# Kernel optimization log

Hardware: AMD Instinct MI355X
Metric: run time of the kernel (lower is better)

## Reference

```python
import jax, jax.numpy as jnp
import numpy as np

D = 1024
H = 16
K = D // H
B = 2
S = 2048

def setup_inputs() -> dict:
    key = jax.random.key(0)
    k1, k2, k3, k4, k5 = jax.random.split(key, 5)
    x = jax.random.normal(k1, (B, S, D), dtype=jnp.float32)
    # nn.Linear(d, 3d): weight [3d, d], bias [3d]
    Wqkv = jax.random.normal(k2, (3 * D, D), dtype=jnp.float32) / np.sqrt(D)
    bqkv = jax.random.normal(k3, (3 * D,), dtype=jnp.float32) * 0.01
    Wproj = jax.random.normal(k4, (D, D), dtype=jnp.float32) / np.sqrt(D)
    bproj = jax.random.normal(k5, (D,), dtype=jnp.float32) * 0.01
    return {"x": x, "Wqkv": Wqkv, "bqkv": bqkv, "Wproj": Wproj, "bproj": bproj}

def reference(x, Wqkv, bqkv, Wproj, bproj):
    Bsz, Slen, d = x.shape
    # fused QKV projection: [B,S,3d] -> [B,S,3,H,K] -> (3, B, H, S, K)
    qkv = (jnp.einsum('bsd,ed->bse', x, Wqkv) + bqkv).reshape(Bsz, Slen, 3, H, K)
    q, k, v = jnp.moveaxis(qkv, 2, 0).transpose(0, 1, 3, 2, 4)
    scale = 1.0 / jnp.sqrt(jnp.asarray(K, dtype=x.dtype))
    scores = jnp.einsum('bhqk,bhmk->bhqm', q, k) * scale  # [B,H,S,S]
    a = jax.nn.softmax(scores, axis=-1)
    # dropout is identity in eval mode
    o = jnp.einsum('bhqm,bhmk->bhqk', a, v)  # [B,H,S,K]
    o = o.transpose(0, 2, 1, 3).reshape(Bsz, Slen, d)
    return jnp.einsum('bsd,ed->bse', o, Wproj) + bproj
```

## Files before the change

kernel.cpp:

```cpp
#include <hip/hip_runtime.h>
#include <cstdint>

typedef unsigned short ushort_t;
typedef short short8 __attribute__((ext_vector_type(8)));
typedef float f32x4 __attribute__((ext_vector_type(4)));
typedef float float4v __attribute__((ext_vector_type(4)));
typedef unsigned int uint2v __attribute__((ext_vector_type(2)));
typedef unsigned int uint4v __attribute__((ext_vector_type(4)));

#define DDIM 1024
#define HH 16
#define HEADK 64
#define BB 2
#define SS 2048

#if __has_builtin(__builtin_amdgcn_exp2f)
#define EXP2F(x) __builtin_amdgcn_exp2f(x)
#else
#define EXP2F(x) exp2f(x)
#endif

__device__ __forceinline__ ushort_t f2bf(float f) {
  union { float f; uint32_t u; } c; c.f = f;
  uint32_t u = c.u;
  u += 0x7fffu + ((u >> 16) & 1u);
  return (ushort_t)(u >> 16);
}

__device__ __forceinline__ uint32_t pkbf_trunc(float a, float b) {
  union { float f; uint32_t u; } ca, cb;
  ca.f = a; cb.f = b;
  return __builtin_amdgcn_perm(cb.u, ca.u, 0x07060302);
}

__device__ __forceinline__ uint32_t pkbf_rne(float a, float b) {
  return (uint32_t)f2bf(a) | ((uint32_t)f2bf(b) << 16);
}

__device__ __forceinline__ float bfhi2f(uint32_t u) {
  union { uint32_t u; float f; } c; c.u = u & 0xffff0000u; return c.f;
}
__device__ __forceinline__ float bflo2f(uint32_t u) {
  union { uint32_t u; float f; } c; c.u = u << 16; return c.f;
}

__device__ __forceinline__ void glds16(const ushort_t* gp, ushort_t* lp) {
  __builtin_amdgcn_global_load_lds(
      (const __attribute__((address_space(1))) uint32_t*)gp,
      (__attribute__((address_space(3))) uint32_t*)lp, 16, 0, 0);
}

__global__ void cvt3_kernel(const float* __restrict__ s0, ushort_t* __restrict__ d0, int n0,
                            const float* __restrict__ s1, ushort_t* __restrict__ d1, int n1,
                            const float* __restrict__ s2, ushort_t* __restrict__ d2, int n2) {
  int i = blockIdx.x * blockDim.x + threadIdx.x;
  const float* src; ushort_t* dst; int k;
  if (i < n0) { src = s0; dst = d0; k = i; }
  else if (i < n0 + n1) { src = s1; dst = d1; k = i - n0; }
  else if (i < n0 + n1 + n2) { src = s2; dst = d2; k = i - n0 - n1; }
  else return;
  float4v v = ((const float4v*)src)[k];
  uint2v o; o[0] = pkbf_rne(v[0], v[1]); o[1] = pkbf_rne(v[2], v[3]);
  ((uint2v*)dst)[k] = o;
}

__global__ __launch_bounds__(512, 2) void gemm_qkv(
    const ushort_t* __restrict__ A, const ushort_t* __restrict__ Bm,
    const float* __restrict__ bias, ushort_t* __restrict__ Cbf) {
  constexpr int Kd = 1024;
  __shared__ ushort_t smem[65536];
  const int tid = threadIdx.x;
  const int wv = tid >> 6, lane = tid & 63;
  const int l15 = lane & 15, quad = lane >> 4;
  const int wm = wv >> 2, wn = wv & 3;
  const int tm0 = blockIdx.y * 256, tn0 = blockIdx.x * 256;
  const int lrow = lane >> 3;
  const int gcb = (lane & 7) ^ lrow;

  f32x4 acc[8][4];
#pragma unroll
  for (int i = 0; i < 8; ++i)
#pragma unroll
    for (int j = 0; j < 4; ++j) acc[i][j] = (f32x4){0.f, 0.f, 0.f, 0.f};

  auto stage = [&](int t, int buf) {
    ushort_t* As = smem + buf * 32768;
    ushort_t* Bs = As + 16384;
    const int k0 = t * 64;
#pragma unroll
    for (int c = 0; c < 4; ++c) {
      int seg = wv * 4 + c;
      glds16(A + (size_t)(tm0 + seg * 8 + lrow) * Kd + k0 + gcb * 8,
             As + seg * 512);
      glds16(Bm + (size_t)(tn0 + seg * 8 + lrow) * Kd + k0 + gcb * 8,
             Bs + seg * 512);
    }
  };

  stage(0, 0);
  for (int t = 0; t < 16; ++t) {
    const int cur = t & 1;
    asm volatile("" ::: "memory");
    __builtin_amdgcn_s_barrier();
    if (t + 1 < 16) {
      stage(t + 1, cur ^ 1);
      asm volatile("s_waitcnt vmcnt(8)" ::: "memory");
    } else {
      asm volatile("s_waitcnt vmcnt(0)" ::: "memory");
    }
    __builtin_amdgcn_s_barrier();
    asm volatile("" ::: "memory");
    __builtin_amdgcn_sched_barrier(0);

    const ushort_t* As = smem + cur * 32768;
    const ushort_t* Bs = As + 16384;
    short8 bfr[4][2];
#pragma unroll
    for (int j = 0; j < 4; ++j)
#pragma unroll
      for (int kc = 0; kc < 2; ++kc) {
        int n = wn * 64 + j * 16 + l15;
        bfr[j][kc] =
            *(const short8*)(Bs + n * 64 + (((kc * 4 + quad) ^ (l15 & 7)) << 3));
      }
#pragma unroll
    for (int q = 0; q < 4; ++q) {
      short8 af[2][2];
#pragma unroll
      for (int i2 = 0; i2 < 2; ++i2)
#pragma unroll
        for (int kc = 0; kc < 2; ++kc) {
          int r = wm * 128 + (q * 2 + i2) * 16 + l15;
          af[i2][kc] =
              *(const short8*)(As + r * 64 + (((kc * 4 + quad) ^ (l15 & 7)) << 3));
        }
      __builtin_amdgcn_s_setprio(1);
#pragma unroll
      for (int kc = 0; kc < 2; ++kc)
#pragma unroll
        for (int i2 = 0; i2 < 2; ++i2)
#pragma unroll
          for (int j = 0; j < 4; ++j)
            acc[q * 2 + i2][j] = __builtin_amdgcn_mfma_f32_16x16x32_bf16(
                af[i2][kc], bfr[j][kc], acc[q * 2 + i2][j], 0, 0, 0);
      __builtin_amdgcn_s_setprio(0);
    }
  }

  const int tsel = tn0 >> 10;
  if (tsel < 2) {
#pragma unroll
    for (int j = 0; j < 4; ++j) {
      int col = tn0 + wn * 64 + j * 16 + l15;
      float bv = bias[col];
      int hh = (col >> 6) & 15, kk2 = col & 63;
#pragma unroll
      for (int mi = 0; mi < 8; ++mi) {
        int row0 = tm0 + wm * 128 + mi * 16 + quad * 4;
#pragma unroll
        for (int r = 0; r < 4; ++r) {
          int row = row0 + r;
          int b = row >> 11, s = row & 2047;
          float v = acc[mi][j][r] + bv;
          if (tsel == 0) v *= 0.18033688f;
          size_t base = (((size_t)tsel * BB + b) * HH + hh) * ((size_t)SS * HEADK);
          Cbf[base + (size_t)s * HEADK + kk2] = f2bf(v);
        }
      }
    }
  } else {
    __builtin_amdgcn_s_barrier();
    ushort_t* slab = smem + wv * 8192;
#pragma unroll
    for (int j = 0; j < 4; ++j) {
      int c = j * 16 + l15;
      float bv = bias[tn0 + wn * 64 + c];
#pragma unroll
      for (int mi = 0; mi < 8; ++mi) {
        int row0 = mi * 16 + quad * 4;
        uint2v dw;
        dw[0] = pkbf_rne(acc[mi][j][0] + bv, acc[mi][j][1] + bv);
        dw[1] = pkbf_rne(acc[mi][j][2] + bv, acc[mi][j][3] + bv);
        int rb = row0 >> 3;
        *(uint2v*)(&slab[c * 128 + (((rb ^ (c & 15)) << 3) | (row0 & 7))]) = dw;
      }
    }
    const int r2 = lane & 15, cg = lane >> 4;
#pragma unroll
    for (int it = 0; it < 16; ++it) {
      int c = it * 4 + cg;
      short8 vv = *(const short8*)(&slab[c * 128 + ((r2 ^ (c & 15)) << 3)]);
      int gcol = tn0 + wn * 64 + c;
      int hh = (gcol >> 6) & 15, kk2 = gcol & 63;
      int grow = tm0 + wm * 128 + r2 * 8;
      int b = grow >> 11, s = grow & 2047;
      size_t base = (((size_t)2 * BB + b) * HH + hh) * ((size_t)SS * HEADK);
      *(short8*)(&Cbf[base + (size_t)kk2 * SS + s]) = vv;
    }
  }
}

__global__ __launch_bounds__(512, 2) void gemm_proj(
    const ushort_t* __restrict__ Op0, const ushort_t* __restrict__ Op1,
    const float* __restrict__ Lp, const ushort_t* __restrict__ Bm,
    const float* __restrict__ bias, float* __restrict__ Cout) {
  constexpr int Kd = 1024;
  constexpr size_t nsL = (size_t)BB * HH * SS;
  __shared__ ushort_t smem[32768];
  const int tid = threadIdx.x;
  const int wv = tid >> 6, lane = tid & 63;
  const int l15 = lane & 15, quad = lane >> 4;
  const int wm = wv >> 2, wn = wv & 3;
  const int tm0 = blockIdx.y * 128, tn0 = blockIdx.x * 128;
  const int lrow = lane >> 3, gcb = (lane & 7) ^ lrow;

  const int ar = tid >> 2, acg = tid & 3;
  const int grow = tm0 + ar;
  const int ab = grow >> 11, as_ = grow & 2047;

  f32x4 acc[4][2];
#pragma unroll
  for (int i = 0; i < 4; ++i)
#pragma unroll
    for (int j = 0; j < 2; ++j) acc[i][j] = (f32x4){0.f, 0.f, 0.f, 0.f};

  uint4v ra0, ra1, rb0, rb1;
  float rl0, rl1;

  auto readA = [&](int t) {
    size_t lo = (size_t)(ab * HH + t) * SS + as_;
    size_t po = lo * 64 + acg * 16;
    ra0 = *(const uint4v*)(Op0 + po);
    ra1 = *(const uint4v*)(Op0 + po + 8);
    rb0 = *(const uint4v*)(Op1 + po);
    rb1 = *(const uint4v*)(Op1 + po + 8);
    rl0 = Lp[lo];
    rl1 = Lp[nsL + lo];
  };
  auto writeA = [&](int p) {
    float inv = 1.0f / (rl0 + rl1);
    uint4v olo, ohi;
#pragma unroll
    for (int d = 0; d < 4; ++d) {
      olo[d] = pkbf_rne((bflo2f(ra0[d]) + bflo2f(rb0[d])) * inv,
                        (bfhi2f(ra0[d]) + bfhi2f(rb0[d])) * inv);
      ohi[d] = pkbf_rne((bflo2f(ra1[d]) + bflo2f(rb1[d])) * inv,
                        (bfhi2f(ra1[d]) + bfhi2f(rb1[d])) * inv);
    }
    ushort_t* As = smem + p * 16384;
    *(uint4v*)(&As[ar * 64 + (((acg * 2) ^ (ar & 7)) << 3)]) = olo;
    *(uint4v*)(&As[ar * 64 + (((acg * 2 + 1) ^ (ar & 7)) << 3)]) = ohi;
  };
  auto stageB = [&](int t, int p) {
    ushort_t* Bs = smem + p * 16384 + 8192;
#pragma unroll
    for (int c = 0; c < 2; ++c) {
      int seg = wv * 2 + c;
      glds16(Bm + (size_t)(tn0 + seg * 8 + lrow) * Kd + t * 64 + gcb * 8,
             Bs + seg * 512);
    }
  };

  readA(0);
  __builtin_amdgcn_sched_barrier(0);
  stageB(0, 0);
  __builtin_amdgcn_sched_barrier(0);
  asm volatile("s_waitcnt vmcnt(2)" ::: "memory");
  writeA(0);

  for (int t = 0; t < 16; ++t) {
    const int p = t & 1;
    asm volatile("s_waitcnt lgkmcnt(0)" ::: "memory");
    __builtin_amdgcn_s_barrier();
    __builtin_amdgcn_sched_barrier(0);
    if (t + 1 < 16) {
      readA(t + 1);
      __builtin_amdgcn_sched_barrier(0);
      stageB(t + 1, p ^ 1);
      __builtin_amdgcn_sched_barrier(0);
      asm volatile("s_waitcnt vmcnt(8)" ::: "memory");
    } else {
      asm volatile("s_waitcnt vmcnt(0)" ::: "memory");
    }
    __builtin_amdgcn_s_barrier();
    asm volatile("" ::: "memory");
    __builtin_amdgcn_sched_barrier(0);

    const ushort_t* As = smem + p * 16384;
    const ushort_t* Bs = As + 8192;
    short8 bfr[2][2], af[4][2];
#pragma unroll
    for (int j = 0; j < 2; ++j)
#pragma unroll
      for (int kc = 0; kc < 2; ++kc) {
        int n = wn * 32 + j * 16 + l15;
        bfr[j][kc] =
            *(const short8*)(Bs + n * 64 + (((kc * 4 + quad) ^ (l15 & 7)) << 3));
      }
#pragma unroll
    for (int mi = 0; mi < 4; ++mi)
#pragma unroll
      for (int kc = 0; kc < 2; ++kc) {
        int r = wm * 64 + mi * 16 + l15;
        af[mi][kc] =
            *(const short8*)(As + r * 64 + (((kc * 4 + quad) ^ (l15 & 7)) << 3));
      }
    __builtin_amdgcn_s_setprio(1);
#pragma unroll
    for (int kc = 0; kc < 2; ++kc)
#pragma unroll
      for (int mi = 0; mi < 4; ++mi)
#pragma unroll
        for (int j = 0; j < 2; ++j)
          acc[mi][j] = __builtin_amdgcn_mfma_f32_16x16x32_bf16(
              af[mi][kc], bfr[j][kc], acc[mi][j], 0, 0, 0);
    __builtin_amdgcn_s_setprio(0);

    if (t + 1 < 16) writeA(p ^ 1);
  }

#pragma unroll
  for (int j = 0; j < 2; ++j) {
    int col = tn0 + wn * 32 + j * 16 + l15;
    float bv = bias[col];
#pragma unroll
    for (int mi = 0; mi < 4; ++mi) {
      int row0 = tm0 + wm * 64 + mi * 16 + quad * 4;
#pragma unroll
      for (int r = 0; r < 4; ++r)
        Cout[(size_t)(row0 + r) * 1024 + col] = acc[mi][j][r] + bv;
    }
  }
}

template <int NSPLIT>
__global__ __launch_bounds__(256, 4) void attn_kernel(
    const ushort_t* __restrict__ qkv, ushort_t* __restrict__ O0,
    ushort_t* __restrict__ O1, float* __restrict__ Lp) {
  constexpr int NT = (SS / NSPLIT) / 32;
  __shared__ ushort_t Kt[3][32 * 64];
  __shared__ ushort_t Vt[3][64 * 32];
  __shared__ ushort_t Pw[4][2][32 * 32];

  const int lin = blockIdx.x + 16 * (blockIdx.y + 16 * blockIdx.z);
  const int xcd = lin & 7, ii = lin >> 3;
  const int qt = ii & 15;
  const int hz = (ii >> 4) * 8 + xcd;
  const int h = hz & 15;
  const int z = hz >> 4;
  const int b = z >> 1, ns = z & 1;
  const int tid = threadIdx.x;
  const int wv = tid >> 6, lane = tid & 63;
  const int l15 = lane & 15, quad = lane >> 4;

  const size_t hstride = (size_t)SS * HEADK;
  const ushort_t* Qg = qkv + ((size_t)(0 * BB + b) * HH + h) * hstride;
  const ushort_t* Kg = qkv + ((size_t)(1 * BB + b) * HH + h) * hstride;
  const ushort_t* Vg = qkv + ((size_t)(2 * BB + b) * HH + h) * hstride;
  ushort_t* Opp = ns ? O1 : O0;

  short8 qf[2][2];
#pragma unroll
  for (int mi = 0; mi < 2; ++mi)
#pragma unroll
    for (int kc = 0; kc < 2; ++kc)
      qf[mi][kc] = *(const short8*)(
          Qg + (size_t)(qt * 128 + wv * 32 + mi * 16 + l15) * 64 + kc * 32 +
          quad * 8);

  const short ONE = (short)0x3F80;
  short8 ones = {ONE, ONE, ONE, ONE, ONE, ONE, ONE, ONE};

  f32x4 oat[2][4];
  f32x4 loa[2];
#pragma unroll
  for (int mi = 0; mi < 2; ++mi) {
    loa[mi] = (f32x4){0.f, 0.f, 0.f, 0.f};
#pragma unroll
    for (int c = 0; c < 4; ++c) oat[mi][c] = (f32x4){0.f, 0.f, 0.f, 0.f};
  }

  const int lrow = lane >> 3, gcb = (lane & 7) ^ lrow;
  const int vfl = lane >> 2;
  const int vgb = (lane & 3) ^ ((vfl >> 1) & 3);

  const int pos0 = ns * (SS / NSPLIT);

  auto stage = [&](int jj, int db) {
    glds16(Kg + (size_t)(pos0 + jj * 32 + wv * 8 + lrow) * 64 + gcb * 8,
           &Kt[db][wv * 512]);
    glds16(Vg + (size_t)(wv * 16 + vfl) * SS + pos0 + jj * 32 + vgb * 8,
           &Vt[db][wv * 512]);
  };

  auto qk_phase = [&](int kb, int pb) {
    f32x4 st[2][2];
    __builtin_amdgcn_s_setprio(1);
#pragma unroll
    for (int cf = 0; cf < 2; ++cf) {
      int n = cf * 16 + l15;
      short8 kf0 = *(const short8*)(&Kt[kb][n * 64 + ((quad ^ (n & 7)) << 3)]);
      short8 kf1 =
          *(const short8*)(&Kt[kb][n * 64 + (((quad + 4) ^ (n & 7)) << 3)]);
#pragma unroll
      for (int mi = 0; mi < 2; ++mi) {
        f32x4 z2 = (f32x4){0.f, 0.f, 0.f, 0.f};
        z2 = __builtin_amdgcn_mfma_f32_16x16x32_bf16(kf0, qf[mi][0], z2, 0, 0, 0);
        z2 = __builtin_amdgcn_mfma_f32_16x16x32_bf16(kf1, qf[mi][1], z2, 0, 0, 0);
        st[mi][cf] = z2;
      }
    }
    __builtin_amdgcn_s_setprio(0);
#pragma unroll
    for (int mi = 0; mi < 2; ++mi)
#pragma unroll
      for (int cf = 0; cf < 2; ++cf) {
        float e0 = EXP2F(st[mi][cf][0]);
        float e1 = EXP2F(st[mi][cf][1]);
        float e2 = EXP2F(st[mi][cf][2]);
        float e3 = EXP2F(st[mi][cf][3]);
        uint2v dw;
        dw[0] = pkbf_trunc(e0, e1);
        dw[1] = pkbf_trunc(e2, e3);
        int row = mi * 16 + l15;
        int pbv = 2 * cf + (quad >> 1);
        int pbs = pbv ^ ((l15 >> 1) & 3);
        *(uint2v*)(&Pw[wv][pb][row * 32 + pbs * 8 + (quad & 1) * 4]) = dw;
      }
  };

  stage(0, 0);
  stage(1, 1);

  asm volatile("s_waitcnt vmcnt(2)" ::: "memory");
  __builtin_amdgcn_s_barrier();
  asm volatile("" ::: "memory");
  __builtin_amdgcn_sched_barrier(0);
  qk_phase(0, 0);

  int vb = 0;
  for (int j = 0; j < NT; ++j) {
    const int kb = (vb == 2) ? 0 : vb + 1;
    const int sb = (kb == 2) ? 0 : kb + 1;
    asm volatile("s_waitcnt vmcnt(0)" ::: "memory");
    __builtin_amdgcn_s_barrier();
    asm volatile("" ::: "memory");
    __builtin_amdgcn_sched_barrier(0);

    if (j + 2 < NT) stage(j + 2, sb);
    if (j + 1 < NT) qk_phase(kb, (j + 1) & 1);

    short8 pa[2];
#pragma unroll
    for (int mi = 0; mi < 2; ++mi) {
      int row = mi * 16 + l15;
      pa[mi] = *(const short8*)(&Pw[wv][j & 1][row * 32 +
                                              ((quad ^ ((l15 >> 1) & 3)) << 3)]);
    }
    __builtin_amdgcn_s_setprio(1);
#pragma unroll
    for (int cf = 0; cf < 4; ++cf) {
      short8 vf = *(const short8*)(&Vt[vb][(cf * 16 + l15) * 32 +
                                           ((quad ^ ((l15 >> 1) & 3)) << 3)]);
#pragma unroll
      for (int mi = 0; mi < 2; ++mi)
        oat[mi][cf] = __builtin_amdgcn_mfma_f32_16x16x32_bf16(
            vf, pa[mi], oat[mi][cf], 0, 0, 0);
    }
#pragma unroll
    for (int mi = 0; mi < 2; ++mi)
      loa[mi] = __builtin_amdgcn_mfma_f32_16x16x32_bf16(ones, pa[mi], loa[mi],
                                                        0, 0, 0);
    __builtin_amdgcn_s_setprio(0);

    vb = kb;
  }

  const size_t obase = ((size_t)b * HH + h) * SS * HEADK;
#pragma unroll
  for (int mi = 0; mi < 2; ++mi) {
#pragma unroll
    for (int cf = 0; cf < 4; ++cf) {
      uint2v dw;
      dw[0] = pkbf_rne(oat[mi][cf][0], oat[mi][cf][1]);
      dw[1] = pkbf_rne(oat[mi][cf][2], oat[mi][cf][3]);
      int cb = 2 * cf + (quad >> 1);
      int cbs = cb ^ (l15 & 7);
      *(uint2v*)(&Pw[wv][0][l15 * 64 + cbs * 8 + (quad & 1) * 4]) = dw;
    }
    const int r = lane >> 2;
#pragma unroll
    for (int pass = 0; pass < 2; ++pass) {
      int g = (lane & 3) + 4 * pass;
      short8 ov = *(const short8*)(&Pw[wv][0][r * 64 + ((g ^ (r & 7)) << 3)]);
      int qrow = qt * 128 + wv * 32 + mi * 16 + r;
      *(short8*)(&Opp[obase + (size_t)qrow * 64 + g * 8]) = ov;
    }
    if (quad == 0) {
      int qrow = qt * 128 + wv * 32 + mi * 16 + l15;
      Lp[((size_t)(ns * BB + b) * HH + h) * SS + qrow] = loa[mi][0];
    }
  }
}

extern "C" void kernel_launch(void* const* d_in, const int* in_sizes, int n_in,
                              void* d_out, int out_size, void* d_ws,
                              size_t ws_size, hipStream_t stream) {
  const float* x = (const float*)d_in[0];
  const float* Wqkv = (const float*)d_in[1];
  const float* bqkv = (const float*)d_in[2];
  const float* Wproj = (const float*)d_in[3];
  const float* bproj = (const float*)d_in[4];
  float* out = (float*)d_out;

  ushort_t* xb = (ushort_t*)d_ws;
  ushort_t* wqb = xb + (size_t)4096 * 1024;
  ushort_t* wpb = wqb + (size_t)3072 * 1024;
  ushort_t* qkvb = wpb + (size_t)1024 * 1024;
  ushort_t* Op1 = qkvb + (size_t)3 * BB * HH * SS * HEADK;
  ushort_t* Op0 = xb;
  float* Lp = (float*)wqb;

  const int n0 = 4096 * 1024 / 4, n1 = 3072 * 1024 / 4, n2 = 1024 * 1024 / 4;
  cvt3_kernel<<<(n0 + n1 + n2 + 255) / 256, 256, 0, stream>>>(
      x, xb, n0, Wqkv, wqb, n1, Wproj, wpb, n2);
  gemm_qkv<<<dim3(3072 / 256, 4096 / 256), 512, 0, stream>>>(xb, wqb, bqkv,
                                                             qkvb);
  attn_kernel<2><<<dim3(16, 16, 4), 256, 0, stream>>>(qkvb, Op0, Op1, Lp);
  gemm_proj<<<dim3(1024 / 128, 4096 / 128), 512, 0, stream>>>(
      Op0, Op1, Lp, wpb, bproj, out);
}
```

Baseline: 186.4 us.

## Replace 256x256 pipelined QKV GEMM with simpler 128x128 tile kernel

Rewrites the QKV projection GEMM to use 128x128 tiles with 256 threads and a single shared-memory buffer, launching four times as many blocks. The goal is to fill all compute units, since the 256-wide tiling produced fewer blocks than CUs. In exchange it drops the double-buffered global-to-LDS prefetch and setprio scheduling, and lowers per-block data reuse, so load latency is hidden only by having more resident blocks.

```diff
diff --git a/kernel.cpp b/kernel.cpp
--- a/kernel.cpp
+++ b/kernel.cpp
@@ -64,135 +64,114 @@
   ((uint2v*)dst)[k] = o;
 }
 
-__global__ __launch_bounds__(512, 2) void gemm_qkv(
+__global__ __launch_bounds__(256) void gemm_qkv128(
     const ushort_t* __restrict__ A, const ushort_t* __restrict__ Bm,
     const float* __restrict__ bias, ushort_t* __restrict__ Cbf) {
   constexpr int Kd = 1024;
-  __shared__ ushort_t smem[65536];
+  __shared__ ushort_t smem[128 * 64 * 2];
+  ushort_t* As = smem;
+  ushort_t* Bs = smem + 128 * 64;
   const int tid = threadIdx.x;
   const int wv = tid >> 6, lane = tid & 63;
   const int l15 = lane & 15, quad = lane >> 4;
-  const int wm = wv >> 2, wn = wv & 3;
-  const int tm0 = blockIdx.y * 256, tn0 = blockIdx.x * 256;
+  const int wm = wv >> 1, wn = wv & 1;
+  const int tm0 = blockIdx.y * 128, tn0 = blockIdx.x * 128;
+
+  f32x4 acc[4][4];
+#pragma unroll
+  for (int i = 0; i < 4; ++i)
+#pragma unroll
+    for (int j = 0; j < 4; ++j) acc[i][j] = (f32x4){0.f, 0.f, 0.f, 0.f};
+
   const int lrow = lane >> 3;
   const int gcb = (lane & 7) ^ lrow;
 
-  f32x4 acc[8][4];
-#pragma unroll
-  for (int i = 0; i < 8; ++i)
-#pragma unroll
-    for (int j = 0; j < 4; ++j) acc[i][j] = (f32x4){0.f, 0.f, 0.f, 0.f};
-
-  auto stage = [&](int t, int buf) {
-    ushort_t* As = smem + buf * 32768;
-    ushort_t* Bs = As + 16384;
-    const int k0 = t * 64;
+  for (int k0 = 0; k0 < Kd; k0 += 64) {
 #pragma unroll
     for (int c = 0; c < 4; ++c) {
       int seg = wv * 4 + c;
       glds16(A + (size_t)(tm0 + seg * 8 + lrow) * Kd + k0 + gcb * 8,
              As + seg * 512);
+    }
+#pragma unroll
+    for (int c = 0; c < 4; ++c) {
+      int seg = wv * 4 + c;
       glds16(Bm + (size_t)(tn0 + seg * 8 + lrow) * Kd + k0 + gcb * 8,
              Bs + seg * 512);
     }
-  };
-
-  stage(0, 0);
-  for (int t = 0; t < 16; ++t) {
-    const int cur = t & 1;
-    asm volatile("" ::: "memory");
-    __builtin_amdgcn_s_barrier();
-    if (t + 1 < 16) {
-      stage(t + 1, cur ^ 1);
-      asm volatile("s_waitcnt vmcnt(8)" ::: "memory");
-    } else {
-      asm volatile("s_waitcnt vmcnt(0)" ::: "memory");
-    }
-    __builtin_amdgcn_s_barrier();
-    asm volatile("" ::: "memory");
-    __builtin_amdgcn_sched_barrier(0);
-
-    const ushort_t* As = smem + cur * 32768;
-    const ushort_t* Bs = As + 16384;
-    short8 bfr[4][2];
-#pragma unroll
-    for (int j = 0; j < 4; ++j)
-#pragma unroll
-      for (int kc = 0; kc < 2; ++kc) {
-        int n = wn * 64 + j * 16 + l15;
-        bfr[j][kc] =
-            *(const short8*)(Bs + n * 64 + (((kc * 4 + quad) ^ (l15 & 7)) << 3));
-      }
-#pragma unroll
-    for (int q = 0; q < 4; ++q) {
-      short8 af[2][2];
-#pragma unroll
-      for (int i2 = 0; i2 < 2; ++i2)
-#pragma unroll
-        for (int kc = 0; kc < 2; ++kc) {
-          int r = wm * 128 + (q * 2 + i2) * 16 + l15;
-          af[i2][kc] =
-              *(const short8*)(As + r * 64 + (((kc * 4 + quad) ^ (l15 & 7)) << 3));
-        }
-      __builtin_amdgcn_s_setprio(1);
-#pragma unroll
-      for (int kc = 0; kc < 2; ++kc)
-#pragma unroll
-        for (int i2 = 0; i2 < 2; ++i2)
-#pragma unroll
-          for (int j = 0; j < 4; ++j)
-            acc[q * 2 + i2][j] = __builtin_amdgcn_mfma_f32_16x16x32_bf16(
-                af[i2][kc], bfr[j][kc], acc[q * 2 + i2][j], 0, 0, 0);
-      __builtin_amdgcn_s_setprio(0);
-    }
-  }
-
-  const int tsel = tn0 >> 10;
-  if (tsel < 2) {
+    __syncthreads();
+#pragma unroll
+    for (int kk = 0; kk < 64; kk += 32) {
+      short8 af[4], bfr[4];
+#pragma unroll
+      for (int i = 0; i < 4; ++i) {
+        int r = wm * 64 + i * 16 + l15;
+        int cb = (kk >> 3) + quad;
+        af[i] = *(const short8*)(As + r * 64 + ((cb ^ (l15 & 7)) << 3));
+      }
+#pragma unroll
+      for (int j = 0; j < 4; ++j) {
+        int r = wn * 64 + j * 16 + l15;
+        int cb = (kk >> 3) + quad;
+        bfr[j] = *(const short8*)(Bs + r * 64 + ((cb ^ (l15 & 7)) << 3));
+      }
+#pragma unroll
+      for (int i = 0; i < 4; ++i)
+#pragma unroll
+        for (int j = 0; j < 4; ++j)
+          acc[i][j] = __builtin_amdgcn_mfma_f32_16x16x32_bf16(
+              af[i], bfr[j], acc[i][j], 0, 0, 0);
+    }
+    __syncthreads();
+  }
+
+  const int t = tn0 >> 10;
+  if (t < 2) {
 #pragma unroll
     for (int j = 0; j < 4; ++j) {
       int col = tn0 + wn * 64 + j * 16 + l15;
       float bv = bias[col];
       int hh = (col >> 6) & 15, kk2 = col & 63;
 #pragma unroll
-      for (int mi = 0; mi < 8; ++mi) {
-        int row0 = tm0 + wm * 128 + mi * 16 + quad * 4;
+      for (int i = 0; i < 4; ++i) {
+        int row0 = tm0 + wm * 64 + i * 16 + quad * 4;
 #pragma unroll
         for (int r = 0; r < 4; ++r) {
           int row = row0 + r;
           int b = row >> 11, s = row & 2047;
-          float v = acc[mi][j][r] + bv;
-          if (tsel == 0) v *= 0.18033688f;
-          size_t base = (((size_t)tsel * BB + b) * HH + hh) * ((size_t)SS * HEADK);
+          float v = acc[i][j][r] + bv;
+          if (t == 0) v *= 0.18033688f;
+          size_t base = (((size_t)t * BB + b) * HH + hh) * ((size_t)SS * HEADK);
           Cbf[base + (size_t)s * HEADK + kk2] = f2bf(v);
         }
       }
     }
   } else {
-    __builtin_amdgcn_s_barrier();
-    ushort_t* slab = smem + wv * 8192;
+    __syncthreads();
 #pragma unroll
     for (int j = 0; j < 4; ++j) {
-      int c = j * 16 + l15;
-      float bv = bias[tn0 + wn * 64 + c];
-#pragma unroll
-      for (int mi = 0; mi < 8; ++mi) {
-        int row0 = mi * 16 + quad * 4;
+      int c = wn * 64 + j * 16 + l15;
+      float bv = bias[tn0 + c];
+#pragma unroll
+      for (int i = 0; i < 4; ++i) {
+        int row0 = wm * 64 + i * 16 + quad * 4;
         uint2v dw;
-        dw[0] = pkbf_rne(acc[mi][j][0] + bv, acc[mi][j][1] + bv);
-        dw[1] = pkbf_rne(acc[mi][j][2] + bv, acc[mi][j][3] + bv);
+        dw[0] = pkbf_rne(acc[i][j][0] + bv, acc[i][j][1] + bv);
+        dw[1] = pkbf_rne(acc[i][j][2] + bv, acc[i][j][3] + bv);
         int rb = row0 >> 3;
-        *(uint2v*)(&slab[c * 128 + (((rb ^ (c & 15)) << 3) | (row0 & 7))]) = dw;
-      }
-    }
-    const int r2 = lane & 15, cg = lane >> 4;
-#pragma unroll
-    for (int it = 0; it < 16; ++it) {
-      int c = it * 4 + cg;
-      short8 vv = *(const short8*)(&slab[c * 128 + ((r2 ^ (c & 15)) << 3)]);
-      int gcol = tn0 + wn * 64 + c;
+        *(uint2v*)(&smem[c * 128 + (((rb ^ (c & 15)) << 3) | (row0 & 7))]) = dw;
+      }
+    }
+    __syncthreads();
+    const int rb2 = lane & 15;
+    const int cg = lane >> 4;
+#pragma unroll
+    for (int it = 0; it < 8; ++it) {
+      int c = wv * 32 + it * 4 + cg;
+      short8 vv = *(const short8*)(&smem[c * 128 + ((rb2 ^ (c & 15)) << 3)]);
+      int gcol = tn0 + c;
       int hh = (gcol >> 6) & 15, kk2 = gcol & 63;
-      int grow = tm0 + wm * 128 + r2 * 8;
+      int grow = tm0 + rb2 * 8;
       int b = grow >> 11, s = grow & 2047;
       size_t base = (((size_t)2 * BB + b) * HH + hh) * ((size_t)SS * HEADK);
       *(short8*)(&Cbf[base + (size_t)kk2 * SS + s]) = vv;
@@ -524,8 +503,8 @@
   const int n0 = 4096 * 1024 / 4, n1 = 3072 * 1024 / 4, n2 = 1024 * 1024 / 4;
   cvt3_kernel<<<(n0 + n1 + n2 + 255) / 256, 256, 0, stream>>>(
       x, xb, n0, Wqkv, wqb, n1, Wproj, wpb, n2);
-  gemm_qkv<<<dim3(3072 / 256, 4096 / 256), 512, 0, stream>>>(xb, wqb, bqkv,
-                                                             qkvb);
+  gemm_qkv128<<<dim3(3072 / 128, 4096 / 128), 256, 0, stream>>>(xb, wqb, bqkv,
+                                                                qkvb);
   attn_kernel<2><<<dim3(16, 16, 4), 256, 0, stream>>>(qkvb, Op0, Op1, Lp);
   gemm_proj<<<dim3(1024 / 128, 4096 / 128), 512, 0, stream>>>(
       Op0, Op1, Lp, wpb, bproj, out);
```

After: 193.6 us. 1.04x slower.
